# Kernel optimization log

Hardware: AMD Instinct MI355X
Metric: run time of the kernel (lower is better)

## Reference

```python
import jax, jax.numpy as jnp
import numpy as np

K = 20
EPS = 1e-5
N = 4096


def lrelu(x):
    return jnp.where(x >= 0, x, 0.2 * x)


def bn(x, g, b, m, v):
    # eval-mode BatchNorm over channel dim 1
    shape = [1] * x.ndim
    shape[1] = -1
    inv = g / jnp.sqrt(v + EPS)
    return (x - m.reshape(shape)) * inv.reshape(shape) + b.reshape(shape)


def get_graph_feature(x):
    # Faithful to repo: num_points = x.shape[1], remaining dims fold into channels.
    p = x.shape[1]
    x2d = x.reshape(-1, p)              # (C, P)
    xx = jnp.sum(x2d * x2d, axis=0)     # (P,)
    dist = 2.0 * (x2d.T @ x2d) - xx[:, None] - xx[None, :]  # -||xi-xj||^2, (P, P)
    idx = jax.lax.top_k(dist, K)[1]     # (P, K) nearest neighbors (incl. self)
    xt = x2d.T                          # (P, C)
    feat = xt[idx]                      # (P, K, C) neighbor gather
    ctr = jnp.broadcast_to(xt[:, None, :], feat.shape)
    out = jnp.concatenate([feat - ctr, ctr], axis=-1)  # (P, K, 2C)
    return out.transpose(2, 0, 1)[None]                # (1, 2C, P, K)


def setup_inputs():
    key = jax.random.key(0)
    ks = jax.random.split(key, 16)

    def w(k_, o, c):
        return jax.random.normal(k_, (o, c), jnp.float32) / float(np.sqrt(c))

    def bnp(k_, c):
        k1, k2, k3, k4 = jax.random.split(k_, 4)
        return (1.0 + 0.1 * jax.random.normal(k1, (c,), jnp.float32),
                0.1 * jax.random.normal(k2, (c,), jnp.float32),
                0.1 * jax.random.normal(k3, (c,), jnp.float32),
                jax.random.uniform(k4, (c,), jnp.float32, minval=0.5, maxval=1.5))

    g1, b1, m1, v1 = bnp(ks[1], 64)
    g2, b2, m2, v2 = bnp(ks[2], 64)
    g3, b3, m3, v3 = bnp(ks[3], 128)
    g4, b4, m4, v4 = bnp(ks[4], 256)
    g5, b5, m5, v5 = bnp(ks[5], 512)
    return dict(
        x=jax.random.normal(ks[0], (3, N), jnp.float32),
        w1=w(ks[6], 64, 6), g1=g1, b1=b1, m1=m1, v1=v1,
        w2=w(ks[7], 64, 64), g2=g2, b2=b2, m2=m2, v2=v2,
        w3=w(ks[8], 128, 64), g3=g3, b3=b3, m3=m3, v3=v3,
        w4=w(ks[9], 256, 128), g4=g4, b4=b4, m4=m4, v4=v4,
        w5=w(ks[10], 512, 256), g5=g5, b5=b5, m5=m5, v5=v5,
        lw1=w(ks[11], 512, 1024),
        lw2=w(ks[12], 256, 512),
        lb2=0.1 * jax.random.normal(ks[13], (256,), jnp.float32),
        ow=w(ks[14], 11, 256),
        ob=0.1 * jax.random.normal(ks[15], (11,), jnp.float32),
    )


def reference(x, w1, g1, b1, m1, v1, w2, g2, b2, m2, v2, w3, g3, b3, m3, v3,
              w4, g4, b4, m4, v4, w5, g5, b5, m5, v5, lw1, lw2, lb2, ow, ob):
    conv2d = lambda w_, f_: jnp.einsum('oc,bcpk->bopk', w_, f_)

    f = get_graph_feature(x)                                   # (1, 6, N, K)
    h = lrelu(bn(conv2d(w1, f), g1, b1, m1, v1))
    x1 = jnp.max(h, axis=-1)                                   # (1, 64, N)

    f = jnp.swapaxes(get_graph_feature(x1), 1, 2)              # (1, 64, 2N, K)
    h = lrelu(bn(conv2d(w2, f), g2, b2, m2, v2))
    x2 = jnp.max(h, axis=-1)                                   # (1, 64, 2N)

    f = jnp.swapaxes(get_graph_feature(x2), 1, 2)              # (1, 64, 4N, K)
    h = lrelu(bn(conv2d(w3, f), g3, b3, m3, v3))
    x3 = jnp.max(h, axis=-1)                                   # (1, 128, 4N)

    f = jnp.swapaxes(get_graph_feature(x3), 1, 2)              # (1, 128, 8N, K)
    h = lrelu(bn(conv2d(w4, f), g4, b4, m4, v4))
    x4 = jnp.max(h, axis=-1)                                   # (1, 256, 8N)

    h5 = lrelu(bn(jnp.einsum('oc,bcp->bop', w5, x4), g5, b5, m5, v5))  # (1, 512, 8N)
    pmax = jnp.max(h5, axis=-1)
    pavg = jnp.mean(h5, axis=-1)
    z = jnp.concatenate([pmax, pavg], axis=1)                  # (1, 1024)
    z = lrelu(z @ lw1.T)                                       # (1, 512); dropout = eval identity
    z = lrelu(z @ lw2.T + lb2)                                 # (1, 256)
    logits = z @ ow.T + ob                                     # (1, 11)
    return jax.nn.softmax(logits, axis=1)
```

## Files before the change

### kernel.cpp

```cpp
#include <hip/hip_runtime.h>
#include <hip/hip_bf16.h>
#include <float.h>
#include <math.h>

#define DEV __device__ __forceinline__

DEV float lrelu(float x) { return x >= 0.f ? x : 0.2f * x; }

constexpr int N = 4096, KNN = 20;

typedef __attribute__((ext_vector_type(4))) float f32x4;
typedef __attribute__((ext_vector_type(8))) short s16x8;

constexpr size_t OFF_SC1 = 0,    OFF_SH1 = 64;
constexpr size_t OFF_SC2 = 128,  OFF_SH2 = 192;
constexpr size_t OFF_SC3 = 256,  OFF_SH3 = 384;
constexpr size_t OFF_SC4 = 512,  OFF_SH4 = 768;
constexpr size_t OFF_SC5 = 1024, OFF_SH5 = 1536;
constexpr size_t OFF_X1 = 2048;
constexpr size_t OFF_X2 = OFF_X1 + (size_t)64*4096;
constexpr size_t OFF_X3 = OFF_X2 + (size_t)64*8192;
constexpr size_t OFF_X4 = OFF_X3 + (size_t)128*16384;
constexpr size_t OFF_A  = OFF_X4 + (size_t)256*32768;
constexpr size_t OFF_GP = OFF_A + (size_t)256*21*128;
constexpr size_t OFF_PM = OFF_GP + (size_t)64*128*128;
constexpr size_t OFF_PS = OFF_PM + (size_t)512*256;
constexpr size_t OFF_Z0 = OFF_PS + (size_t)512*256;
constexpr size_t OFF_Z1 = OFF_Z0 + 1024;
constexpr size_t OFF_Z2 = OFF_Z1 + 512;
constexpr size_t OFF_IDX = OFF_Z2 + 256;
constexpr size_t WS_NEEDED_BYTES = OFF_IDX * 4 + (size_t)N * KNN * 4;
constexpr size_t OFF_ABF = OFF_A;
constexpr size_t OFF_W5BF = OFF_A + 524288;

__global__ void k_ws_sentinel(float* out, float mb) {
  int t = threadIdx.x;
  if (t < 11) out[t] = 1.0e6f + mb;
}

__global__ __launch_bounds__(512) void k_bn_pre(
    const float* g1, const float* b1, const float* m1, const float* v1,
    const float* g2, const float* b2, const float* m2, const float* v2,
    const float* g3, const float* b3, const float* m3, const float* v3,
    const float* g4, const float* b4, const float* m4, const float* v4,
    const float* g5, const float* b5, const float* m5, const float* v5,
    float* ws) {
  int t = threadIdx.x;
  const float* G[5] = {g1,g2,g3,g4,g5};
  const float* B[5] = {b1,b2,b3,b4,b5};
  const float* M[5] = {m1,m2,m3,m4,m5};
  const float* V[5] = {v1,v2,v3,v4,v5};
  const size_t SC[5] = {OFF_SC1,OFF_SC2,OFF_SC3,OFF_SC4,OFF_SC5};
  const size_t SH[5] = {OFF_SH1,OFF_SH2,OFF_SH3,OFF_SH4,OFF_SH5};
  const int CN[5] = {64,64,128,256,512};
  for (int s = 0; s < 5; ++s) {
    for (int i = t; i < CN[s]; i += 512) {
      float scale = G[s][i] / sqrtf(V[s][i] + 1e-5f);
      ws[SC[s] + i] = scale;
      ws[SH[s] + i] = B[s][i] - M[s][i] * scale;
    }
  }
}

__global__ __launch_bounds__(256) void k_s1_topk(const float* x, int* idx) {
  __shared__ float d[N];
  __shared__ float wls[4];
  __shared__ int wis[4];
  int i = blockIdx.x, t = threadIdx.x;
  {
    #pragma clang fp contract(off)
    float xi0 = x[i], xi1 = x[N + i], xi2 = x[2*N + i];
    float sqi = xi0*xi0 + xi1*xi1 + xi2*xi2;
    for (int j = t; j < N; j += 256) {
      float xj0 = x[j], xj1 = x[N+j], xj2 = x[2*N+j];
      float sqj = xj0*xj0 + xj1*xj1 + xj2*xj2;
      float p = xi0*xj0 + xi1*xj1 + xi2*xj2;
      d[j] = (2.f*p - sqi) - sqj;
    }
  }
  __syncthreads();
  int lane = t & 63, wid = t >> 6;
  float bv = -FLT_MAX; int bi = N;
  for (int j = t; j < N; j += 256) { float v = d[j]; if (v > bv) { bv = v; bi = j; } }
  for (int k = 0; k < KNN; ++k) {
    float rv = bv; int ri = bi;
    #pragma unroll
    for (int off = 1; off < 64; off <<= 1) {
      float v2 = __shfl_xor(rv, off); int i2 = __shfl_xor(ri, off);
      if (v2 > rv || (v2 == rv && i2 < ri)) { rv = v2; ri = i2; }
    }
    if (lane == 0) { wls[wid] = rv; wis[wid] = ri; }
    __syncthreads();
    float fv = wls[0]; int fi = wis[0];
    #pragma unroll
    for (int w2 = 1; w2 < 4; ++w2) {
      float v2 = wls[w2]; int i2 = wis[w2];
      if (v2 > fv || (v2 == fv && i2 < fi)) { fv = v2; fi = i2; }
    }
    if (t == 0) idx[i*KNN + k] = fi;
    if ((fi & 255) == t) {
      d[fi] = -FLT_MAX;
      bv = -FLT_MAX; bi = N;
      for (int j = t; j < N; j += 256) { float v = d[j]; if (v > bv) { bv = v; bi = j; } }
    }
    __syncthreads();
  }
}

__global__ __launch_bounds__(256) void k_s1_conv(const float* x, const float* w1g,
                                                 const int* idx, const float* sc, const float* sh, float* x1) {
  __shared__ int idxs[64][KNN];
  __shared__ float xs[3][64];
  __shared__ float wsh[4][6];
  int t = threadIdx.x, bx = blockIdx.x, by = blockIdx.y;
  int i0 = bx * 64;
  for (int u = t; u < 64*KNN; u += 256) idxs[u/KNN][u%KNN] = idx[(size_t)(i0 + u/KNN)*KNN + u%KNN];
  for (int u = t; u < 3*64; u += 256) xs[u/64][u%64] = x[(size_t)(u/64)*N + i0 + (u%64)];
  for (int u = t; u < 24; u += 256) wsh[u/6][u%6] = w1g[(size_t)(by*4 + u/6)*6 + u%6];
  __syncthreads();
  int il = t & 63, ol = t >> 6;
  int o = by*4 + ol, i = i0 + il;
  float xi0 = xs[0][il], xi1 = xs[1][il], xi2 = xs[2][il];
  float w0 = wsh[ol][0], w1v = wsh[ol][1], w2v = wsh[ol][2];
  float w3v = wsh[ol][3], w4v = wsh[ol][4], w5v = wsh[ol][5];
  float ctr = w3v*xi0 + w4v*xi1 + w5v*xi2;
  float scale = sc[o], shift = sh[o];
  float best = -FLT_MAX;
  for (int k = 0; k < KNN; ++k) {
    int j = idxs[il][k];
    float h = w0*(x[j] - xi0) + w1v*(x[N+j] - xi1) + w2v*(x[2*N+j] - xi2) + ctr;
    h = lrelu(h*scale + shift);
    best = fmaxf(best, h);
  }
  x1[(size_t)o*N + i] = best;
}

template<int P>
__global__ __launch_bounds__(256) void k_gram_partial(const float* prev, int C, float* gp) {
  constexpr int BI = P / 16;
  __shared__ float ysh[32][P];
  int b = blockIdx.x, t = threadIdx.x;
  int R = C / gridDim.x;
  int base = b * R;
  float acc[BI][BI] = {};
  int i0 = (t >> 4) * BI, j0 = (t & 15) * BI;
  for (int r0 = 0; r0 < R; r0 += 32) {
    for (int u = t; u < 32*P; u += 256) ysh[u/P][u%P] = prev[(size_t)(base + r0 + u/P)*P + (u%P)];
    __syncthreads();
    for (int r = 0; r < 32; ++r) {
      float yi[BI], yj[BI];
      #pragma unroll
      for (int a = 0; a < BI; ++a) { yi[a] = ysh[r][i0+a]; yj[a] = ysh[r][j0+a]; }
      #pragma unroll
      for (int a = 0; a < BI; ++a)
        #pragma unroll
        for (int c = 0; c < BI; ++c) acc[a][c] += yi[a]*yj[c];
    }
    __syncthreads();
  }
  for (int a = 0; a < BI; ++a)
    for (int c = 0; c < BI; ++c)
      gp[(size_t)b*P*P + (size_t)(i0+a)*P + (j0+c)] = acc[a][c];
}

template<int P>
__global__ __launch_bounds__(128) void k_dist_topk(const float* gp, int* idx, int nb) {
  __shared__ float dsh[P];
  __shared__ float diag[P];
  __shared__ float vsh[128];
  __shared__ int ish[128];
  int i = blockIdx.x, t = threadIdx.x;
  if (t < P) {
    int q = nb >> 2;
    float g0 = 0.f, g1 = 0.f, g2 = 0.f, g3 = 0.f;
    float e0 = 0.f, e1 = 0.f, e2 = 0.f, e3 = 0.f;
    for (int b = 0; b < q; ++b) {
      size_t o0 = (size_t)b*P*P, o1 = (size_t)(b+q)*P*P, o2 = (size_t)(b+2*q)*P*P, o3 = (size_t)(b+3*q)*P*P;
      g0 += gp[o0 + (size_t)i*P + t]; g1 += gp[o1 + (size_t)i*P + t];
      g2 += gp[o2 + (size_t)i*P + t]; g3 += gp[o3 + (size_t)i*P + t];
      e0 += gp[o0 + (size_t)t*P + t]; e1 += gp[o1 + (size_t)t*P + t];
      e2 += gp[o2 + (size_t)t*P + t]; e3 += gp[o3 + (size_t)t*P + t];
    }
    diag[t] = (e0 + e1) + (e2 + e3);
    dsh[t] = (g0 + g1) + (g2 + g3);
  }
  __syncthreads();
  if (t < P) dsh[t] = (2.f*dsh[t] - diag[i]) - diag[t];
  __syncthreads();
  for (int k = 0; k < KNN; ++k) {
    float bv = -FLT_MAX; int bi = P;
    if (t < P) { bv = dsh[t]; bi = t; }
    vsh[t] = bv; ish[t] = bi;
    __syncthreads();
    for (int s = 64; s > 0; s >>= 1) {
      if (t < s) {
        float v2 = vsh[t+s]; int i2 = ish[t+s];
        if (v2 > vsh[t] || (v2 == vsh[t] && i2 < ish[t])) { vsh[t] = v2; ish[t] = i2; }
      }
      __syncthreads();
    }
    if (t == 0) { idx[i*KNN + k] = ish[0]; dsh[ish[0]] = -FLT_MAX; }
    __syncthreads();
  }
}

template<int P>
__global__ __launch_bounds__(64) void k_build_A(const float* w, const int* idx, int O, float* A) {
  __shared__ float row[64][P];
  int t = threadIdx.x;
  int r = blockIdx.x*64 + t;
  if (r < O*21) {
    int o = r / 21, kk = r % 21;
    float* my = row[t];
    if (kk == 20) {
      for (int i2 = 0; i2 < P; ++i2) my[i2] = w[(size_t)o*P + i2];
    } else {
      for (int i2 = 0; i2 < P; ++i2) my[i2] = 0.f;
      for (int j = 0; j < P; ++j) my[idx[j*KNN + kk]] += w[(size_t)o*P + j];
    }
    for (int i2 = 0; i2 < P; ++i2) A[(size_t)r*P + i2] = my[i2];
  }
}

__global__ __launch_bounds__(64) void k_build_A_bf(const float* w, const int* idx, __hip_bfloat16* A) {
  __shared__ float row[64][128];
  int t = threadIdx.x;
  int r = blockIdx.x*64 + t;
  int o = r >> 5, kk = r & 31;
  float* my = row[t];
  if (kk == 20) {
    for (int i2 = 0; i2 < 128; ++i2) my[i2] = w[(size_t)o*128 + i2];
  } else if (kk < 20) {
    for (int i2 = 0; i2 < 128; ++i2) my[i2] = 0.f;
    for (int j = 0; j < 128; ++j) my[idx[j*KNN + kk]] += w[(size_t)o*128 + j];
  } else {
    for (int i2 = 0; i2 < 128; ++i2) my[i2] = 0.f;
  }
  for (int i2 = 0; i2 < 128; ++i2) A[(size_t)r*128 + i2] = __float2bfloat16(my[i2]);
}

__global__ __launch_bounds__(256) void k_f32_to_bf16(const float* in, __hip_bfloat16* out) {
  size_t base = ((size_t)blockIdx.x*256 + threadIdx.x) * 16;
  #pragma unroll
  for (int j = 0; j < 4; ++j) {
    float4 v = *(const float4*)(in + base + j*4);
    __hip_bfloat16 tmp[4] = {__float2bfloat16(v.x), __float2bfloat16(v.y),
                             __float2bfloat16(v.z), __float2bfloat16(v.w)};
    *(ushort4*)(out + base + j*4) = *(const ushort4*)tmp;
  }
}

__global__ __launch_bounds__(512, 2) void k_conv4_mfma(const __hip_bfloat16* Abf, const __hip_bfloat16* Xbf,
                                                       const float* sc, const float* sh, float* x4) {
  constexpr int MT = 256;
  __shared__ char Bs[MT*256];
  int t = threadIdx.x, bx = blockIdx.x, byg = blockIdx.y;
  int m0 = bx*MT;
  for (int u = t; u < MT*16; u += 512) {
    int row = u >> 4, k8 = u & 15;
    s16x8 v = *(const s16x8*)(Xbf + ((size_t)(m0+row) << 7) + (k8 << 3));
    *(s16x8*)(Bs + (row << 8) + ((k8 << 4) ^ ((row & 7) << 4))) = v;
  }
  __syncthreads();
  int lane = t & 63, w = t >> 6;
  int col = lane & 15, lg = lane >> 4;
  int q = w & 3, pb = w >> 2;
  for (int it = 0; it < 8; ++it) {
    int by = byg*16 + it*2 + pb;
    const __hip_bfloat16* Ab = Abf + ((size_t)(by*64) << 7);
    f32x4 acc[4][4] = {};
    #pragma unroll
    for (int ks = 0; ks < 4; ++ks) {
      int kel = ks*32 + lg*8;
      int kbyte = ks*64 + lg*16;
      s16x8 a[4], b[4];
      #pragma unroll
      for (int at = 0; at < 4; ++at)
        a[at] = *(const s16x8*)(Ab + ((size_t)(at*16 + col) << 7) + kel);
      #pragma unroll
      for (int bt = 0; bt < 4; ++bt) {
        int r = q*64 + bt*16 + col;
        b[bt] = *(const s16x8*)(Bs + (r << 8) + (kbyte ^ ((r & 7) << 4)));
      }
      #pragma unroll
      for (int at = 0; at < 4; ++at)
        #pragma unroll
        for (int bt = 0; bt < 4; ++bt)
          acc[at][bt] = __builtin_amdgcn_mfma_f32_16x16x32_bf16(a[at], b[bt], acc[at][bt], 0, 0, 0);
    }
    int o0 = by*2;
    #pragma unroll
    for (int ol = 0; ol < 2; ++ol) {
      float scale = sc[o0+ol], shift = sh[o0+ol];
      float mxv[4], ctv[4];
      #pragma unroll
      for (int bt = 0; bt < 4; ++bt) {
        float h2b = __shfl(acc[2*ol+1][bt][0], 16 + col);
        float mx = -FLT_MAX;
        #pragma unroll
        for (int qq = 0; qq < 4; ++qq) {
          mx = fmaxf(mx, lrelu((acc[2*ol][bt][qq] - h2b)*scale + shift));
          float v1 = lrelu((acc[2*ol+1][bt][qq] - h2b)*scale + shift);
          if (lg == 0) mx = fmaxf(mx, v1);
        }
        mx = fmaxf(mx, __shfl_xor(mx, 16));
        mx = fmaxf(mx, __shfl_xor(mx, 32));
        mxv[bt] = mx;
        ctv[bt] = lrelu(h2b*scale + shift);
      }
      float vb = (lg == 0) ? mxv[0] : (lg == 1) ? mxv[1] : (lg == 2) ? mxv[2] : mxv[3];
      float vc = (lg == 0) ? ctv[0] : (lg == 1) ? ctv[1] : (lg == 2) ? ctv[2] : ctv[3];
      size_t pbase = (size_t)(o0+ol)*32768 + m0 + q*64 + lane;
      x4[pbase] = vb;
      x4[pbase + 16384] = vc;
    }
  }
}

template<int P>
__global__ __launch_bounds__(256) void k_fused_conv(const float* prev, const float* A,
                                                    const float* sc, const float* sh,
                                                    int C, float* outx) {
  constexpr int TO = 8, ROWS = TO*21;
  __shared__ float Ash[ROWS][65];
  __shared__ float Bsh[64][132];
  int bx = blockIdx.x, by = blockIdx.y, t = threadIdx.x;
  int m0 = bx*128;
  int rowbase = by*ROWS;
  int ol = t >> 5, mg = t & 31;
  float acc[21][4] = {};
  for (int ic = 0; ic < P/64; ++ic) {
    for (int u = t; u < ROWS*64; u += 256) {
      int rr = u >> 6, cc = u & 63;
      Ash[rr][cc] = A[(size_t)(rowbase + rr)*P + ic*64 + cc];
    }
    for (int u = t; u < 64*128; u += 256) {
      int mr = u >> 6, ii = u & 63;
      Bsh[ii][mr] = prev[(size_t)(m0 + mr)*P + ic*64 + ii];
    }
    __syncthreads();
    for (int i = 0; i < 64; ++i) {
      float v0 = Bsh[i][mg*4+0], v1 = Bsh[i][mg*4+1], v2 = Bsh[i][mg*4+2], v3 = Bsh[i][mg*4+3];
      #pragma unroll
      for (int kk = 0; kk < 21; ++kk) {
        float a = Ash[ol*21 + kk][i];
        acc[kk][0] += a*v0; acc[kk][1] += a*v1; acc[kk][2] += a*v2; acc[kk][3] += a*v3;
      }
    }
    __syncthreads();
  }
  int o = by*TO + ol;
  float scale = sc[o], shift = sh[o];
  size_t C2 = 2*(size_t)C;
  #pragma unroll
  for (int mm = 0; mm < 4; ++mm) {
    int m = m0 + mg*4 + mm;
    float h2 = acc[20][mm];
    float ctr = lrelu(h2*scale + shift);
    float best = -FLT_MAX;
    #pragma unroll
    for (int kk = 0; kk < 20; ++kk) {
      float v = lrelu((acc[kk][mm] - h2)*scale + shift);
      best = fmaxf(best, v);
    }
    outx[(size_t)o*C2 + m] = best;
    outx[(size_t)o*C2 + C + m] = ctr;
  }
}

__global__ __launch_bounds__(256) void k_s5_mfma(const float* x4, const __hip_bfloat16* w5bf,
                                                 const float* sc, const float* sh,
                                                 float* pm, float* ps) {
  __shared__ char smem[8192 + 32768];
  __shared__ float redm[64][4];
  __shared__ float reds[64][4];
  int t = threadIdx.x, bx = blockIdx.x, by = blockIdx.y;
  int p0 = bx*256, o0 = by*64;
  int lane = t & 63, w = t >> 6;
  int lrow = lane & 15, lg = lane >> 4;
  char* As = smem;
  char* Bs = smem + 8192;
  f32x4 acc[4][4] = {};
  for (int c0 = 0; c0 < 256; c0 += 64) {
    for (int u = t; u < 64*8; u += 256) {
      int row = u >> 3, k8 = u & 7;
      s16x8 v = *(const s16x8*)(w5bf + (size_t)(o0+row)*256 + c0 + k8*8);
      *(s16x8*)(As + row*128 + ((k8*16) ^ ((row&7)<<4))) = v;
    }
    #pragma unroll
    for (int i = 0; i < 8; ++i) {
      __hip_bfloat16 tmp[8];
      #pragma unroll
      for (int j = 0; j < 8; ++j)
        tmp[j] = __float2bfloat16(x4[(size_t)(c0 + i*8 + j)*32768 + p0 + t]);
      *(s16x8*)(Bs + t*128 + ((i*16) ^ ((t&7)<<4))) = *(const s16x8*)tmp;
    }
    __syncthreads();
    #pragma unroll
    for (int ksub = 0; ksub < 2; ++ksub) {
      int kbyte = ksub*64 + lg*16;
      s16x8 a[4], b[4];
      #pragma unroll
      for (int rt = 0; rt < 4; ++rt) { int r = rt*16 + lrow; a[rt] = *(const s16x8*)(As + r*128 + (kbyte ^ ((r&7)<<4))); }
      #pragma unroll
      for (int cf = 0; cf < 4; ++cf) { int r = w*64 + cf*16 + lrow; b[cf] = *(const s16x8*)(Bs + r*128 + (kbyte ^ ((r&7)<<4))); }
      #pragma unroll
      for (int rt = 0; rt < 4; ++rt)
        #pragma unroll
        for (int cf = 0; cf < 4; ++cf)
          acc[rt][cf] = __builtin_amdgcn_mfma_f32_16x16x32_bf16(a[rt], b[cf], acc[rt][cf], 0, 0, 0);
    }
    __syncthreads();
  }
  #pragma unroll
  for (int rt = 0; rt < 4; ++rt) {
    #pragma unroll
    for (int q = 0; q < 4; ++q) {
      int ol = rt*16 + lg*4 + q;
      float scale = sc[o0+ol], shift = sh[o0+ol];
      float mx = -FLT_MAX, sm = 0.f;
      #pragma unroll
      for (int cf = 0; cf < 4; ++cf) {
        float h = lrelu(acc[rt][cf][q]*scale + shift);
        mx = fmaxf(mx, h); sm += h;
      }
      #pragma unroll
      for (int off2 = 1; off2 < 16; off2 <<= 1) {
        mx = fmaxf(mx, __shfl_xor(mx, off2));
        sm += __shfl_xor(sm, off2);
      }
      if (lrow == 0) { redm[ol][w] = mx; reds[ol][w] = sm; }
    }
  }
  __syncthreads();
  if (t < 64) {
    float mx = fmaxf(fmaxf(redm[t][0], redm[t][1]), fmaxf(redm[t][2], redm[t][3]));
    float sm = reds[t][0] + reds[t][1] + reds[t][2] + reds[t][3];
    pm[(size_t)(o0 + t)*128 + bx] = mx;
    ps[(size_t)(o0 + t)*128 + bx] = sm;
  }
}

__global__ __launch_bounds__(512) void k_pool(const float* pm, const float* ps, float* z0) {
  int t = threadIdx.x;
  for (int o = t; o < 512; o += 512) {
    float mx = -FLT_MAX, sm = 0.f;
    for (int nt = 0; nt < 128; ++nt) { mx = fmaxf(mx, pm[(size_t)o*128+nt]); sm += ps[(size_t)o*128+nt]; }
    z0[o] = mx;
    z0[512+o] = sm * (1.f/32768.f);
  }
}

__global__ __launch_bounds__(128) void k_fc1(const float* z0, const float* lw1, float* z1) {
  int bx = blockIdx.x, t = threadIdx.x;
  int rl = t >> 4, cl = t & 15;
  int r = bx*8 + rl;
  float acc = 0.f;
  for (int u = 0; u < 64; ++u) {
    int c = cl*64 + u;
    acc += z0[c] * lw1[(size_t)r*1024 + c];
  }
  #pragma unroll
  for (int off = 1; off < 16; off <<= 1) acc += __shfl_xor(acc, off);
  if (cl == 0) z1[r] = lrelu(acc);
}

__global__ __launch_bounds__(128) void k_fc2(const float* z1, const float* lw2,
                                             const float* lb2, float* z2) {
  int bx = blockIdx.x, t = threadIdx.x;
  int rl = t >> 4, cl = t & 15;
  int r = bx*8 + rl;
  float acc = 0.f;
  for (int u = 0; u < 32; ++u) {
    int c = cl*32 + u;
    acc += z1[c] * lw2[(size_t)r*512 + c];
  }
  #pragma unroll
  for (int off = 1; off < 16; off <<= 1) acc += __shfl_xor(acc, off);
  if (cl == 0) z2[r] = lrelu(acc + lb2[r]);
}

__global__ __launch_bounds__(64) void k_fc3(const float* z2, const float* ow,
                                            const float* ob, float* out) {
  __shared__ float lg[11];
  __shared__ float ex[11];
  int t = threadIdx.x;
  if (t < 11) {
    float acc = 0.f;
    for (int c = 0; c < 256; ++c) acc += z2[c] * ow[t*256 + c];
    lg[t] = acc + ob[t];
  }
  __syncthreads();
  if (t < 11) {
    float m = -FLT_MAX;
    for (int r = 0; r < 11; ++r) m = fmaxf(m, lg[r]);
    ex[t] = expf(lg[t] - m);
  }
  __syncthreads();
  if (t < 11) {
    float s = 0.f;
    for (int r = 0; r < 11; ++r) s += ex[r];
    out[t] = ex[t] / s;
  }
}

extern "C" void kernel_launch(void* const* d_in, const int* in_sizes, int n_in,
                              void* d_out, int out_size, void* d_ws, size_t ws_size,
                              hipStream_t stream) {
  auto f = [&](int i) { return (const float*)d_in[i]; };
  float* ws = (float*)d_ws;
  int* idx = (int*)(ws + OFF_IDX);
  float* out = (float*)d_out;

  if (ws_size < WS_NEEDED_BYTES) {
    k_ws_sentinel<<<1, 64, 0, stream>>>(out, (float)(ws_size >> 20));
    return;
  }

  __hip_bfloat16* Abf = (__hip_bfloat16*)(ws + OFF_ABF);
  __hip_bfloat16* Xbf = (__hip_bfloat16*)(ws + OFF_GP);
  __hip_bfloat16* w5bf = (__hip_bfloat16*)(ws + OFF_W5BF);
  float* x4 = ws + OFF_X4;

  k_bn_pre<<<1, 512, 0, stream>>>(f(2),f(3),f(4),f(5), f(7),f(8),f(9),f(10),
                                  f(12),f(13),f(14),f(15), f(17),f(18),f(19),f(20),
                                  f(22),f(23),f(24),f(25), ws);
  k_s1_topk<<<N, 256, 0, stream>>>(f(0), idx);
  k_s1_conv<<<dim3(N/64, 16), 256, 0, stream>>>(f(0), f(1), idx, ws+OFF_SC1, ws+OFF_SH1, ws+OFF_X1);
  k_gram_partial<64><<<64, 256, 0, stream>>>(ws+OFF_X1, 4096, ws+OFF_GP);
  k_dist_topk<64><<<64, 128, 0, stream>>>(ws+OFF_GP, idx, 64);
  k_build_A<64><<<21, 64, 0, stream>>>(f(6), idx, 64, ws+OFF_A);
  k_fused_conv<64><<<dim3(4096/128, 64/8), 256, 0, stream>>>(ws+OFF_X1, ws+OFF_A, ws+OFF_SC2, ws+OFF_SH2, 4096, ws+OFF_X2);
  k_gram_partial<64><<<64, 256, 0, stream>>>(ws+OFF_X2, 8192, ws+OFF_GP);
  k_dist_topk<64><<<64, 128, 0, stream>>>(ws+OFF_GP, idx, 64);
  k_build_A<64><<<42, 64, 0, stream>>>(f(11), idx, 128, ws+OFF_A);
  k_fused_conv<64><<<dim3(8192/128, 128/8), 256, 0, stream>>>(ws+OFF_X2, ws+OFF_A, ws+OFF_SC3, ws+OFF_SH3, 8192, ws+OFF_X3);
  k_gram_partial<128><<<64, 256, 0, stream>>>(ws+OFF_X3, 16384, ws+OFF_GP);
  k_dist_topk<128><<<128, 128, 0, stream>>>(ws+OFF_GP, idx, 64);
  k_build_A_bf<<<128, 64, 0, stream>>>(f(16), idx, Abf);
  k_f32_to_bf16<<<512, 256, 0, stream>>>(ws+OFF_X3, Xbf);
  k_conv4_mfma<<<dim3(16384/256, 8), 512, 0, stream>>>(Abf, Xbf, ws+OFF_SC4, ws+OFF_SH4, x4);
  k_f32_to_bf16<<<32, 256, 0, stream>>>(f(21), w5bf);
  k_s5_mfma<<<dim3(128, 8), 256, 0, stream>>>(x4, w5bf, ws+OFF_SC5, ws+OFF_SH5, ws+OFF_PM, ws+OFF_PS);
  k_pool<<<1, 512, 0, stream>>>(ws+OFF_PM, ws+OFF_PS, ws+OFF_Z0);
  k_fc1<<<64, 128, 0, stream>>>(ws+OFF_Z0, f(26), ws+OFF_Z1);
  k_fc2<<<32, 128, 0, stream>>>(ws+OFF_Z1, f(27), f(28), ws+OFF_Z2);
  k_fc3<<<1, 64, 0, stream>>>(ws+OFF_Z2, f(29), f(30), out);
}
```

Measured before the change: 523.8 us.

## Assign one wavefront per query point in stage-1 top-k using register-resident distances

The stage-1 kNN kernel now handles four query points per block, one per wavefront, keeping each lane's 64 distances in registers instead of a 16KB shared array. Top-k selection uses only wave shuffles, which removes the per-iteration block barriers and the shared-memory cross-wave reduction. The cost is 64 floats of register state per lane, statically indexed through unrolled loops, and each lane rescans all 64 registers whenever it contributes a winner.

```diff
diff --git a/kernel.cpp b/kernel.cpp
--- a/kernel.cpp
+++ b/kernel.cpp
@@ -62,26 +62,30 @@
   }
 }
 
-__global__ __launch_bounds__(256) void k_s1_topk(const float* x, int* idx) {
-  __shared__ float d[N];
-  __shared__ float wls[4];
-  __shared__ int wis[4];
-  int i = blockIdx.x, t = threadIdx.x;
+__global__ __launch_bounds__(256, 4) void k_s1_topk(const float* x, int* idx) {
+  int t = threadIdx.x;
+  int lane = t & 63, wid = t >> 6;
+  int i = blockIdx.x*4 + wid;
+  float v[64];
   {
     #pragma clang fp contract(off)
     float xi0 = x[i], xi1 = x[N + i], xi2 = x[2*N + i];
     float sqi = xi0*xi0 + xi1*xi1 + xi2*xi2;
-    for (int j = t; j < N; j += 256) {
+    #pragma unroll
+    for (int u = 0; u < 64; ++u) {
+      int j = u*64 + lane;
       float xj0 = x[j], xj1 = x[N+j], xj2 = x[2*N+j];
       float sqj = xj0*xj0 + xj1*xj1 + xj2*xj2;
       float p = xi0*xj0 + xi1*xj1 + xi2*xj2;
-      d[j] = (2.f*p - sqi) - sqj;
-    }
-  }
-  __syncthreads();
-  int lane = t & 63, wid = t >> 6;
+      v[u] = (2.f*p - sqi) - sqj;
+    }
+  }
   float bv = -FLT_MAX; int bi = N;
-  for (int j = t; j < N; j += 256) { float v = d[j]; if (v > bv) { bv = v; bi = j; } }
+  #pragma unroll
+  for (int u = 0; u < 64; ++u) {
+    int j = u*64 + lane;
+    if (v[u] > bv) { bv = v[u]; bi = j; }
+  }
   for (int k = 0; k < KNN; ++k) {
     float rv = bv; int ri = bi;
     #pragma unroll
@@ -89,21 +93,17 @@
       float v2 = __shfl_xor(rv, off); int i2 = __shfl_xor(ri, off);
       if (v2 > rv || (v2 == rv && i2 < ri)) { rv = v2; ri = i2; }
     }
-    if (lane == 0) { wls[wid] = rv; wis[wid] = ri; }
-    __syncthreads();
-    float fv = wls[0]; int fi = wis[0];
-    #pragma unroll
-    for (int w2 = 1; w2 < 4; ++w2) {
-      float v2 = wls[w2]; int i2 = wis[w2];
-      if (v2 > fv || (v2 == fv && i2 < fi)) { fv = v2; fi = i2; }
-    }
-    if (t == 0) idx[i*KNN + k] = fi;
-    if ((fi & 255) == t) {
-      d[fi] = -FLT_MAX;
+    if (lane == 0) idx[i*KNN + k] = ri;
+    if ((ri & 63) == lane) {
+      int wu = ri >> 6;
       bv = -FLT_MAX; bi = N;
-      for (int j = t; j < N; j += 256) { float v = d[j]; if (v > bv) { bv = v; bi = j; } }
-    }
-    __syncthreads();
+      #pragma unroll
+      for (int u = 0; u < 64; ++u) {
+        if (u == wu) v[u] = -FLT_MAX;
+        int j = u*64 + lane;
+        if (v[u] > bv) { bv = v[u]; bi = j; }
+      }
+    }
   }
 }
 
@@ -525,7 +525,7 @@
   k_bn_pre<<<1, 512, 0, stream>>>(f(2),f(3),f(4),f(5), f(7),f(8),f(9),f(10),
                                   f(12),f(13),f(14),f(15), f(17),f(18),f(19),f(20),
                                   f(22),f(23),f(24),f(25), ws);
-  k_s1_topk<<<N, 256, 0, stream>>>(f(0), idx);
+  k_s1_topk<<<N/4, 256, 0, stream>>>(f(0), idx);
   k_s1_conv<<<dim3(N/64, 16), 256, 0, stream>>>(f(0), f(1), idx, ws+OFF_SC1, ws+OFF_SH1, ws+OFF_X1);
   k_gram_partial<64><<<64, 256, 0, stream>>>(ws+OFF_X1, 4096, ws+OFF_GP);
   k_dist_topk<64><<<64, 128, 0, stream>>>(ws+OFF_GP, idx, 64);
```

After: 507.0 us. 1.03x faster.
